# Optimization experiments

Measured on AMD Instinct MI355X. Metric: run time of the kernel, lower is better.

## Reference

```python
import jax, jax.numpy as jnp
import numpy as np

FISTA_ITER = 50
LAMBDA = 0.1
POWER_ITER = 100


def power_method(W):
    # Estimates c = largest eigenvalue of W^T W (squared spectral norm).
    # Torch code uses a random init vector; we use a fixed key for determinism.
    X0 = jax.random.normal(jax.random.key(1), (1, W.shape[1]), dtype=W.dtype)

    def body(i, carry):
        X, _ = carry
        X = (X @ W.T) @ W            # [1, m]
        nm = jnp.linalg.norm(X)
        return (X / nm, nm)

    _, nm = jax.lax.fori_loop(0, POWER_ITER, body, (X0, jnp.asarray(1.0, W.dtype)))
    return nm


def soft_threshold(X, lam):
    return jnp.sign(X) * jax.nn.relu(jnp.abs(X) - lam)


def fista(Y, W, lam, iters):
    c = power_method(W)
    eta = 1.0 / c
    Gamma0 = soft_threshold(Y @ (eta * W), lam)   # [B, m]
    Y_norm = jnp.linalg.norm(Y)
    t0 = jnp.asarray(1.0, Y.dtype)

    def step(carry, _):
        Gamma, Z, t = carry
        residual = Z @ W.T - Y                                   # [B, n]
        Gamma_new = soft_threshold(Z - eta * (residual @ W), lam / c)
        t_new = (1.0 + jnp.sqrt(1.0 + 4.0 * t ** 2)) / 2.0
        Z_new = Gamma_new + (t - 1.0) / t_new * (Gamma_new - Gamma)
        nrm = jnp.linalg.norm(residual) / Y_norm
        return (Gamma_new, Z_new, t_new), nrm

    (Gamma, _, _), norms = jax.lax.scan(step, (Gamma0, Gamma0, t0), None, length=iters)
    return Gamma, norms


def setup_inputs() -> dict:
    key = jax.random.key(0)
    k1, k2 = jax.random.split(key)
    Y = jax.random.normal(k1, (8192, 784), dtype=jnp.float32)
    W = jax.random.normal(k2, (784, 2048), dtype=jnp.float32)
    W = W / jnp.linalg.norm(W, axis=0, keepdims=True)  # NormDict
    return {"Y": Y, "W": W}


def reference(Y, W):
    Gamma, norms = fista(Y, W, LAMBDA, FISTA_ITER)
    X = Gamma @ W.T                  # reconstruction [B, 784]
    return (X, Gamma, norms)
```

## Files before the change

### kernel.cpp

```cpp
#include <hip/hip_runtime.h>
#include <math.h>

#define B_DIM   8192
#define N_DIM   784
#define NPAD    800
#define NROWS_W 896
#define M_DIM   2048
#define XSZ     (B_DIM*N_DIM)
#define GSZ     (B_DIM*M_DIM)
#define NITER   50
#define PITER   100

typedef __attribute__((ext_vector_type(8))) short short8;
typedef __attribute__((ext_vector_type(4))) float floatx4;

__device__ __forceinline__ void async_ld16(const unsigned short* g, unsigned short* l){
  __builtin_amdgcn_global_load_lds(
      (const __attribute__((address_space(1))) unsigned int*)g,
      (__attribute__((address_space(3))) unsigned int*)l,
      16, 0, 0);
}

__device__ __forceinline__ unsigned rotl32(unsigned x, int d){ return (x<<d)|(x>>(32-d)); }

__device__ void threefry2x32(unsigned& v0, unsigned& v1){
  const unsigned ks0=0u, ks1=1u, ks2=0x1BD11BDBu;
  unsigned x0=v0+ks0, x1=v1+ks1;
#define RND(R) { x0+=x1; x1=rotl32(x1,R); x1^=x0; }
  RND(13) RND(15) RND(26) RND(6)
  x0+=ks1; x1+=ks2+1u;
  RND(17) RND(29) RND(16) RND(24)
  x0+=ks2; x1+=ks0+2u;
  RND(13) RND(15) RND(26) RND(6)
  x0+=ks0; x1+=ks1+3u;
  RND(17) RND(29) RND(16) RND(24)
  x0+=ks1; x1+=ks2+4u;
  RND(13) RND(15) RND(26) RND(6)
  x0+=ks2; x1+=ks0+5u;
#undef RND
  v0=x0; v1=x1;
}

__device__ float erfinv_f(float x){
  float w = -logf((1.0f-x)*(1.0f+x));
  float p;
  if (w < 5.0f){
    w -= 2.5f;
    p = 2.81022636e-08f;
    p = fmaf(p,w, 3.43273939e-07f);
    p = fmaf(p,w,-3.5233877e-06f);
    p = fmaf(p,w,-4.39150654e-06f);
    p = fmaf(p,w, 0.00021858087f);
    p = fmaf(p,w,-0.00125372503f);
    p = fmaf(p,w,-0.00417768164f);
    p = fmaf(p,w, 0.246640727f);
    p = fmaf(p,w, 1.50140941f);
  } else {
    w = sqrtf(w) - 3.0f;
    p = -0.000200214257f;
    p = fmaf(p,w, 0.000100950558f);
    p = fmaf(p,w, 0.00134934322f);
    p = fmaf(p,w,-0.00367342844f);
    p = fmaf(p,w, 0.00573950773f);
    p = fmaf(p,w,-0.0076224613f);
    p = fmaf(p,w, 0.00943887047f);
    p = fmaf(p,w, 1.00167406f);
    p = fmaf(p,w, 2.83297682f);
  }
  return p*x;
}

__device__ float bits_to_normal(unsigned b){
  unsigned fb = (b>>9) | 0x3f800000u;
  float u01 = __uint_as_float(fb) - 1.0f;
  const float lo = -0.99999994f;
  float u = u01*(1.0f - lo) + lo;
  u = fmaxf(lo, u);
  return 1.41421356237f * erfinv_f(u);
}

__global__ void setup_kernel(float* __restrict__ xbuf0, float* __restrict__ accs){
  int i = threadIdx.x;
  if (i < 64) accs[i] = 0.0f;
  unsigned v0 = (unsigned)i, v1 = (unsigned)(1024+i);
  threefry2x32(v0, v1);
  xbuf0[i]        = bits_to_normal(v0);
  xbuf0[1024 + i] = bits_to_normal(v1);
}

__device__ __forceinline__ unsigned short f2bf(float f){
  unsigned u = __float_as_uint(f);
  unsigned r = (u + 0x7fffu + ((u>>16)&1u)) >> 16;
  return (unsigned short)r;
}
__device__ __forceinline__ unsigned pack2(float a, float b){
  return (unsigned)f2bf(a) | ((unsigned)f2bf(b) << 16);
}
__device__ __forceinline__ float bf2f(unsigned short s){
  return __uint_as_float(((unsigned)s) << 16);
}

__global__ void conv_w(const float* __restrict__ W, unsigned short* __restrict__ Wbf){
  int i4 = (blockIdx.x*256 + threadIdx.x)*4;
  int row = i4 >> 11;
  uint2 p = make_uint2(0,0);
  if (row < N_DIM){
    float4 v = *(const float4*)(W + (size_t)row*M_DIM + (i4 & 2047));
    p.x = pack2(v.x, v.y); p.y = pack2(v.z, v.w);
  }
  *(uint2*)(Wbf + i4) = p;
}

__global__ void conv_y(const float* __restrict__ Y, unsigned short* __restrict__ Ybf){
  int row = blockIdx.x;
  int c4 = threadIdx.x*4;
  if (c4 >= NPAD) return;
  uint2 p = make_uint2(0,0);
  if (c4 < N_DIM){
    float4 v = *(const float4*)(Y + (size_t)row*N_DIM + c4);
    p.x = pack2(v.x, v.y); p.y = pack2(v.z, v.w);
  }
  *(uint2*)(Ybf + (size_t)row*NPAD + c4) = p;
}

__global__ void transpose_w(const float* __restrict__ W, unsigned short* __restrict__ WTbf){
  __shared__ float tile[32][33];
  int k0 = blockIdx.x*32;
  int j0 = blockIdx.y*32;
  int tx = threadIdx.x & 31, ty = threadIdx.x >> 5;
#pragma unroll
  for (int i=0;i<4;i++){
    int j = j0 + ty + 8*i;
    float v = (j < N_DIM) ? W[(size_t)j*M_DIM + k0 + tx] : 0.0f;
    tile[tx][ty+8*i] = v;
  }
  __syncthreads();
#pragma unroll
  for (int i=0;i<4;i++){
    int k = k0 + ty + 8*i;
    WTbf[(size_t)k*NPAD + j0 + tx] = f2bf(tile[ty+8*i][tx]);
  }
}

__global__ __launch_bounds__(256)
void compute_q(const float* __restrict__ W, float* __restrict__ Q){
  __shared__ float As2[16][132];
  __shared__ float Bs2[16][132];
  const int t = threadIdx.x;
  const int a0 = blockIdx.x*128, b0 = blockIdx.y*128;
  const int ty = t>>4, tx = t&15;
  float acc[8][8];
#pragma unroll
  for (int i=0;i<8;i++)
#pragma unroll
    for (int j=0;j<8;j++) acc[i][j]=0.0f;

  for (int j0=0; j0<N_DIM; j0+=16){
#pragma unroll
    for (int h=0; h<8; ++h){
      int idx = h*256 + t;
      int r = idx>>7, c = idx&127;
      As2[r][c] = W[(size_t)(j0+r)*M_DIM + a0 + c];
      Bs2[r][c] = W[(size_t)(j0+r)*M_DIM + b0 + c];
    }
    __syncthreads();
#pragma unroll
    for (int kk=0; kk<16; ++kk){
      float a[8], b[8];
#pragma unroll
      for (int i=0;i<8;i++) a[i] = As2[kk][ty*8+i];
#pragma unroll
      for (int j=0;j<8;j++) b[j] = Bs2[kk][tx*8+j];
#pragma unroll
      for (int i=0;i<8;i++)
#pragma unroll
        for (int j=0;j<8;j++) acc[i][j] = fmaf(a[i], b[j], acc[i][j]);
    }
    __syncthreads();
  }
#pragma unroll
  for (int i=0;i<8;i++){
    int a = a0 + ty*8 + i;
#pragma unroll
    for (int j=0;j<8;j++) Q[(size_t)a*M_DIM + b0 + tx*8 + j] = acc[i][j];
  }
}

__global__ void sumsq_kernel(const float* __restrict__ v, int n, float* __restrict__ acc){
  __shared__ float red[256];
  int t = threadIdx.x;
  float s = 0.0f;
  for (int i = blockIdx.x*256 + t; i < n; i += gridDim.x*256){ float x = v[i]; s = fmaf(x,x,s); }
  red[t] = s; __syncthreads();
  for (int off=128; off>0; off>>=1){ if (t<off) red[t]+=red[t+off]; __syncthreads(); }
  if (t==0) atomicAdd(acc, red[0]);
}

__global__ void pm_q(const float* __restrict__ x, const float* __restrict__ Q,
                     float* __restrict__ xout){
  __shared__ float red[256];
  int t = threadIdx.x;
  float s = 0.0f;
  for (int k=t; k<M_DIM; k+=256){ float v = x[k]; s = fmaf(v,v,s); }
  red[t]=s; __syncthreads();
  for (int off=128; off>0; off>>=1){ if (t<off) red[t]+=red[t+off]; __syncthreads(); }
  float inv = 1.0f/sqrtf(red[0]);
  int wave = t>>6, lane = t&63;
  int j = blockIdx.x*4 + wave;
  const float* Qr = Q + (size_t)j*M_DIM;
  float acc = 0.0f;
  for (int k=lane; k<M_DIM; k+=64) acc = fmaf(x[k], Qr[k], acc);
  for (int off=32; off>0; off>>=1) acc += __shfl_down(acc, off);
  if (lane==0) xout[j] = acc * inv;
}

__global__ void finish_power(const float* __restrict__ xfin, const float* __restrict__ accs,
                             float* __restrict__ params){
  __shared__ float red[256];
  int t = threadIdx.x;
  float s = 0.0f;
  for (int k=t; k<M_DIM; k+=256){ float v = xfin[k]; s = fmaf(v,v,s); }
  red[t]=s; __syncthreads();
  for (int off=128; off>0; off>>=1){ if (t<off) red[t]+=red[t+off]; __syncthreads(); }
  if (t==0){
    float c = sqrtf(red[0]);
    params[0] = c;
    params[1] = 1.0f/c;
    params[2] = 0.1f/c;
    params[3] = sqrtf(accs[0]);
  }
}

__device__ __forceinline__ float softthr(float v, float th){
  float a = fmaxf(fabsf(v) - th, 0.0f);
  return copysignf(a, v);
}

template<int MODE>
__global__ __launch_bounds__(256)
void mfma_nt(const unsigned short* __restrict__ Abf,
             const unsigned short* __restrict__ Bbf,
             const float* __restrict__ Y,
             unsigned short* __restrict__ Rbf,
             float* __restrict__ X,
             float* __restrict__ nacc){
  __shared__ float4 smem4[1024];
  unsigned short* As = (unsigned short*)smem4;
  unsigned short* Bs = As + 64*32;
  float* fbuf = (float*)smem4;

  const int bid = blockIdx.x;
  const int g8  = bid & 7, w = bid >> 3;
  const int mt  = w / 7, nt = w - mt*7;
  const int m0  = (g8*16 + mt)*64;
  const int n0  = nt*128;

  const int t    = threadIdx.x;
  const int wave = t>>6, lane = t&63;
  const int wm2  = wave>>1, wn2 = wave&1;
  const int quad = lane>>4, l15 = lane&15;
  const int lrow = lane>>2;
  const int lk   = (lane&3)*8;

  floatx4 acc[2][4];
#pragma unroll
  for (int i=0;i<2;i++)
#pragma unroll
    for (int j=0;j<4;j++) acc[i][j] = (floatx4)(0.0f);

  for (int k0=0; k0<M_DIM; k0+=32){
    async_ld16(Abf + (size_t)(m0 + wave*16 + lrow)*M_DIM + k0 + lk, &As[wave*512]);
#pragma unroll
    for (int c=0; c<2; ++c){
      int chunk = wave*2 + c;
      async_ld16(Bbf + (size_t)(n0 + chunk*16 + lrow)*M_DIM + k0 + lk, &Bs[chunk*512]);
    }
    __syncthreads();
    short8 af[2], bfr[4];
#pragma unroll
    for (int ti=0; ti<2; ++ti)
      af[ti] = *(const short8*)&As[(wm2*32 + ti*16 + l15)*32 + quad*8];
#pragma unroll
    for (int tj=0; tj<4; ++tj)
      bfr[tj] = *(const short8*)&Bs[(wn2*64 + tj*16 + l15)*32 + quad*8];
#pragma unroll
    for (int ti=0; ti<2; ++ti)
#pragma unroll
      for (int tj=0; tj<4; ++tj)
        acc[ti][tj] = __builtin_amdgcn_mfma_f32_16x16x32_bf16(af[ti], bfr[tj], acc[ti][tj], 0, 0, 0);
    __syncthreads();
  }

  float ss = 0.0f;
#pragma unroll
  for (int c=0; c<2; ++c){
    if (wn2 == c){
#pragma unroll
      for (int ti=0; ti<2; ++ti)
#pragma unroll
        for (int tj=0; tj<4; ++tj)
#pragma unroll
          for (int r=0; r<4; ++r)
            fbuf[(wm2*32 + ti*16 + quad*4 + r)*64 + tj*16 + l15] = acc[ti][tj][r];
    }
    __syncthreads();
#pragma unroll
    for (int k=0; k<4; ++k){
      int row = k*16 + (t>>4);
      int col = (t&15)*4;
      int m = m0 + row;
      int n = n0 + c*64 + col;
      float4 v = *(const float4*)&fbuf[row*64 + col];
      if (MODE==0){
        if (n < N_DIM){
          float4 yv = *(const float4*)(Y + (size_t)m*N_DIM + n);
          float r0 = v.x - yv.x, r1 = v.y - yv.y, r2 = v.z - yv.z, r3 = v.w - yv.w;
          uint2 p; p.x = pack2(r0, r1); p.y = pack2(r2, r3);
          *(uint2*)(Rbf + (size_t)m*NPAD + n) = p;
          ss = fmaf(r0,r0, fmaf(r1,r1, fmaf(r2,r2, fmaf(r3,r3, ss))));
        } else if (n < NPAD){
          *(uint2*)(Rbf + (size_t)m*NPAD + n) = make_uint2(0,0);
        }
      } else {
        if (n < N_DIM) *(float4*)(X + (size_t)m*N_DIM + n) = v;
      }
    }
    __syncthreads();
  }

  if (MODE==0){
    for (int off=32; off>0; off>>=1) ss += __shfl_down(ss, off);
    if (lane==0) atomicAdd(nacc, ss);
  }
}

template<int MODE>
__global__ __launch_bounds__(256)
void mfma_nn(const unsigned short* __restrict__ Abf,
             const unsigned short* __restrict__ WTbf,
             float* __restrict__ Gamma,
             unsigned short* __restrict__ Zhi,
             unsigned short* __restrict__ Zlo,
             const float* __restrict__ params,
             float mu){
  __shared__ float4 smem4[1024];
  unsigned short* As = (unsigned short*)smem4;
  unsigned short* Bs = As + 128*32;
  float* fbuf = (float*)smem4;

  const int bid = blockIdx.x;
  const int g8  = bid & 7, w = bid >> 3;
  const int m0  = (g8*8 + (w>>4))*128;
  const int n0  = (w & 15)*128;

  const int t    = threadIdx.x;
  const int wave = t>>6, lane = t&63;
  const int wm   = wave>>1, wn = wave&1;
  const int quad = lane>>4, l15 = lane&15;
  const int ch0  = wave*2;
  const int lrow = lane>>2;
  const int lk   = (lane&3)*8;

  floatx4 acc[4][4];
#pragma unroll
  for (int i=0;i<4;i++)
#pragma unroll
    for (int j=0;j<4;j++) acc[i][j] = (floatx4)(0.0f);

  for (int k0=0; k0<NPAD; k0+=32){
#pragma unroll
    for (int c=0; c<2; ++c){
      int chunk = ch0 + c;
      async_ld16(Abf  + (size_t)(m0 + chunk*16 + lrow)*NPAD + k0 + lk, &As[chunk*512]);
      async_ld16(WTbf + (size_t)(n0 + chunk*16 + lrow)*NPAD + k0 + lk, &Bs[chunk*512]);
    }
    __syncthreads();
    short8 af[4], bfr[4];
#pragma unroll
    for (int ti=0; ti<4; ++ti)
      af[ti] = *(const short8*)&As[(wm*64 + ti*16 + l15)*32 + quad*8];
#pragma unroll
    for (int tj=0; tj<4; ++tj)
      bfr[tj] = *(const short8*)&Bs[(wn*64 + tj*16 + l15)*32 + quad*8];
#pragma unroll
    for (int ti=0; ti<4; ++ti)
#pragma unroll
      for (int tj=0; tj<4; ++tj)
        acc[ti][tj] = __builtin_amdgcn_mfma_f32_16x16x32_bf16(af[ti], bfr[tj], acc[ti][tj], 0, 0, 0);
    __syncthreads();
  }

  const float eta  = params[1];
  const float lamc = params[2];

#pragma unroll
  for (int c=0; c<4; ++c){
    if (wn == (c>>1)){
      int tjb = (c&1)*2;
#pragma unroll
      for (int ti=0; ti<4; ++ti)
#pragma unroll
        for (int u=0; u<2; ++u)
#pragma unroll
          for (int r=0; r<4; ++r)
            fbuf[(wm*64 + ti*16 + quad*4 + r)*32 + u*16 + l15] = acc[ti][tjb+u][r];
    }
    __syncthreads();
#pragma unroll
    for (int k=0; k<4; ++k){
      int row = k*32 + (t>>3);
      int col = (t&7)*4;
      int m = m0 + row;
      int n = n0 + c*32 + col;
      size_t idx = (size_t)m*M_DIM + n;
      float4 g4 = *(const float4*)&fbuf[row*32 + col];
      float gr[4] = {g4.x, g4.y, g4.z, g4.w};
      float go4[4];
      if (MODE!=0){
        uint2 ph = *(const uint2*)(Zhi + idx);
        uint2 pl = *(const uint2*)(Zlo + idx);
        unsigned short h[4] = {(unsigned short)(ph.x&0xffff),(unsigned short)(ph.x>>16),
                               (unsigned short)(ph.y&0xffff),(unsigned short)(ph.y>>16)};
        unsigned short l[4] = {(unsigned short)(pl.x&0xffff),(unsigned short)(pl.x>>16),
                               (unsigned short)(pl.y&0xffff),(unsigned short)(pl.y>>16)};
        float4 gov = *(const float4*)(Gamma + idx);
        go4[0]=gov.x; go4[1]=gov.y; go4[2]=gov.z; go4[3]=gov.w;
#pragma unroll
        for (int e=0;e<4;e++){
          float zv = bf2f(h[e]) + bf2f(l[e]);
          gr[e] = softthr(zv - eta*gr[e], lamc);
        }
      } else {
#pragma unroll
        for (int e=0;e<4;e++) gr[e] = softthr(eta*gr[e], 0.1f);
      }
      *(float4*)(Gamma + idx) = make_float4(gr[0],gr[1],gr[2],gr[3]);
      if (MODE==1){
        float zn[4];
#pragma unroll
        for (int e=0;e<4;e++) zn[e] = gr[e] + mu*(gr[e] - go4[e]);
        unsigned short h0=f2bf(zn[0]), h1=f2bf(zn[1]), h2=f2bf(zn[2]), h3=f2bf(zn[3]);
        uint2 ph; ph.x = (unsigned)h0 | ((unsigned)h1<<16); ph.y = (unsigned)h2 | ((unsigned)h3<<16);
        uint2 pl; pl.x = pack2(zn[0]-bf2f(h0), zn[1]-bf2f(h1));
                  pl.y = pack2(zn[2]-bf2f(h2), zn[3]-bf2f(h3));
        *(uint2*)(Zhi + idx) = ph;
        *(uint2*)(Zlo + idx) = pl;
      } else if (MODE==0){
        unsigned short h0=f2bf(gr[0]), h1=f2bf(gr[1]), h2=f2bf(gr[2]), h3=f2bf(gr[3]);
        uint2 ph; ph.x = (unsigned)h0 | ((unsigned)h1<<16); ph.y = (unsigned)h2 | ((unsigned)h3<<16);
        uint2 pl; pl.x = pack2(gr[0]-bf2f(h0), gr[1]-bf2f(h1));
                  pl.y = pack2(gr[2]-bf2f(h2), gr[3]-bf2f(h3));
        *(uint2*)(Zhi + idx) = ph;
        *(uint2*)(Zlo + idx) = pl;
      } else {
        uint2 ph; ph.x = pack2(gr[0], gr[1]); ph.y = pack2(gr[2], gr[3]);
        *(uint2*)(Zhi + idx) = ph;
      }
    }
    __syncthreads();
  }
}

__global__ void norms_finalize(const float* __restrict__ nacc, const float* __restrict__ params,
                               float* __restrict__ out){
  int i = threadIdx.x;
  if (i < NITER) out[i] = sqrtf(nacc[i]) / params[3];
}

extern "C" void kernel_launch(void* const* d_in, const int* in_sizes, int n_in,
                              void* d_out, int out_size, void* d_ws, size_t ws_size,
                              hipStream_t stream){
  const float* Y  = (const float*)d_in[0];
  const float* W  = (const float*)d_in[1];
  float* out      = (float*)d_out;
  float* X        = out;
  float* Gamma    = out + XSZ;
  float* norms    = out + XSZ + GSZ;

  unsigned short* Zhi  = (unsigned short*)d_ws;
  unsigned short* Zlo  = Zhi  + (size_t)GSZ;
  unsigned short* Rbf  = Zlo  + (size_t)GSZ;
  unsigned short* Wbf  = Rbf  + (size_t)B_DIM*NPAD;
  unsigned short* WTbf = Wbf  + (size_t)NROWS_W*M_DIM;
  float* Q      = (float*)(WTbf + (size_t)M_DIM*NPAD);
  float* xb0    = Q + (size_t)M_DIM*M_DIM;
  float* xb1    = xb0 + M_DIM;
  float* params = xb1 + M_DIM;
  float* accs   = params + 8;

  setup_kernel<<<dim3(1), dim3(1024), 0, stream>>>(xb0, accs);
  sumsq_kernel<<<dim3(512), dim3(256), 0, stream>>>(Y, XSZ, accs);
  conv_w      <<<dim3(1792), dim3(256), 0, stream>>>(W, Wbf);
  transpose_w <<<dim3(64,25), dim3(256), 0, stream>>>(W, WTbf);
  conv_y      <<<dim3(B_DIM), dim3(256), 0, stream>>>(Y, Rbf);

  compute_q<<<dim3(16,16), dim3(256), 0, stream>>>(W, Q);
  float* xa = xb0; float* xc = xb1;
  for (int it=0; it<PITER; ++it){
    pm_q<<<dim3(512), dim3(256), 0, stream>>>(xa, Q, xc);
    float* tmp = xa; xa = xc; xc = tmp;
  }
  finish_power<<<dim3(1), dim3(256), 0, stream>>>(xa, accs, params);

  mfma_nn<0><<<dim3(1024), dim3(256), 0, stream>>>(Rbf, WTbf, Gamma, Zhi, Zlo, params, 0.0f);

  float tcur = 1.0f;
  for (int it=0; it<NITER; ++it){
    mfma_nt<0><<<dim3(896), dim3(256), 0, stream>>>(Zhi, Wbf, Y, Rbf, nullptr, accs + 1 + it);
    float tsq = tcur*tcur;
    float tn  = (1.0f + sqrtf(1.0f + 4.0f*tsq)) / 2.0f;
    float mu  = (tcur - 1.0f) / tn;
    tcur = tn;
    if (it < NITER-1)
      mfma_nn<1><<<dim3(1024), dim3(256), 0, stream>>>(Rbf, WTbf, Gamma, Zhi, Zlo, params, mu);
    else
      mfma_nn<2><<<dim3(1024), dim3(256), 0, stream>>>(Rbf, WTbf, Gamma, Zhi, Zlo, params, mu);
  }

  norms_finalize<<<dim3(1), dim3(64), 0, stream>>>(accs + 1, params, norms);

  mfma_nt<1><<<dim3(896), dim3(256), 0, stream>>>(Zhi, Wbf, nullptr, nullptr, X, nullptr);
}
```

Measured before the change: 9.500 ms.

## Square the Gram matrix for power iteration and narrow mfma_nn tiles

Computes Q² = (WᵀW)² once and runs the power method with half as many matrix-vector launches, bracketed by single Q applications. Separately, shrinks the FISTA gradient GEMM tile from 128x128 to 128x64, doubling the grid and requesting higher occupancy via launch bounds. The squaring adds a large fp32 SIMT GEMM up front and slightly changes iteration count and normalization; the smaller tile lowers per-block reuse in exchange for more parallelism.

Measured after the change: 9.727 ms. +2.4%, slower.

```diff
diff --git a/kernel.cpp b/kernel.cpp
--- a/kernel.cpp
+++ b/kernel.cpp
@@ -142,8 +142,9 @@
   }
 }
 
+template<int KROWS>
 __global__ __launch_bounds__(256)
-void compute_q(const float* __restrict__ W, float* __restrict__ Q){
+void compute_qk(const float* __restrict__ A, float* __restrict__ Qout){
   __shared__ float As2[16][132];
   __shared__ float Bs2[16][132];
   const int t = threadIdx.x;
@@ -155,13 +156,13 @@
 #pragma unroll
     for (int j=0;j<8;j++) acc[i][j]=0.0f;
 
-  for (int j0=0; j0<N_DIM; j0+=16){
+  for (int j0=0; j0<KROWS; j0+=16){
 #pragma unroll
     for (int h=0; h<8; ++h){
       int idx = h*256 + t;
       int r = idx>>7, c = idx&127;
-      As2[r][c] = W[(size_t)(j0+r)*M_DIM + a0 + c];
-      Bs2[r][c] = W[(size_t)(j0+r)*M_DIM + b0 + c];
+      As2[r][c] = A[(size_t)(j0+r)*M_DIM + a0 + c];
+      Bs2[r][c] = A[(size_t)(j0+r)*M_DIM + b0 + c];
     }
     __syncthreads();
 #pragma unroll
@@ -182,7 +183,7 @@
   for (int i=0;i<8;i++){
     int a = a0 + ty*8 + i;
 #pragma unroll
-    for (int j=0;j<8;j++) Q[(size_t)a*M_DIM + b0 + tx*8 + j] = acc[i][j];
+    for (int j=0;j<8;j++) Qout[(size_t)a*M_DIM + b0 + tx*8 + j] = acc[i][j];
   }
 }
 
@@ -196,7 +197,7 @@
   if (t==0) atomicAdd(acc, red[0]);
 }
 
-__global__ void pm_q(const float* __restrict__ x, const float* __restrict__ Q,
+__global__ void pm_q(const float* __restrict__ x, const float* __restrict__ M,
                      float* __restrict__ xout){
   __shared__ float red[256];
   int t = threadIdx.x;
@@ -207,9 +208,9 @@
   float inv = 1.0f/sqrtf(red[0]);
   int wave = t>>6, lane = t&63;
   int j = blockIdx.x*4 + wave;
-  const float* Qr = Q + (size_t)j*M_DIM;
+  const float* Mr = M + (size_t)j*M_DIM;
   float acc = 0.0f;
-  for (int k=lane; k<M_DIM; k+=64) acc = fmaf(x[k], Qr[k], acc);
+  for (int k=lane; k<M_DIM; k+=64) acc = fmaf(x[k], Mr[k], acc);
   for (int off=32; off>0; off>>=1) acc += __shfl_down(acc, off);
   if (lane==0) xout[j] = acc * inv;
 }
@@ -335,7 +336,7 @@
 }
 
 template<int MODE>
-__global__ __launch_bounds__(256)
+__global__ __launch_bounds__(256, 5)
 void mfma_nn(const unsigned short* __restrict__ Abf,
              const unsigned short* __restrict__ WTbf,
              float* __restrict__ Gamma,
@@ -350,42 +351,41 @@
 
   const int bid = blockIdx.x;
   const int g8  = bid & 7, w = bid >> 3;
-  const int m0  = (g8*8 + (w>>4))*128;
-  const int n0  = (w & 15)*128;
+  const int m0  = (g8*8 + (w>>5))*128;
+  const int n0  = (w & 31)*64;
 
   const int t    = threadIdx.x;
   const int wave = t>>6, lane = t&63;
   const int wm   = wave>>1, wn = wave&1;
   const int quad = lane>>4, l15 = lane&15;
-  const int ch0  = wave*2;
   const int lrow = lane>>2;
   const int lk   = (lane&3)*8;
 
-  floatx4 acc[4][4];
+  floatx4 acc[4][2];
 #pragma unroll
   for (int i=0;i<4;i++)
 #pragma unroll
-    for (int j=0;j<4;j++) acc[i][j] = (floatx4)(0.0f);
+    for (int j=0;j<2;j++) acc[i][j] = (floatx4)(0.0f);
 
   for (int k0=0; k0<NPAD; k0+=32){
 #pragma unroll
     for (int c=0; c<2; ++c){
-      int chunk = ch0 + c;
-      async_ld16(Abf  + (size_t)(m0 + chunk*16 + lrow)*NPAD + k0 + lk, &As[chunk*512]);
-      async_ld16(WTbf + (size_t)(n0 + chunk*16 + lrow)*NPAD + k0 + lk, &Bs[chunk*512]);
-    }
-    __syncthreads();
-    short8 af[4], bfr[4];
+      int chunk = wave*2 + c;
+      async_ld16(Abf + (size_t)(m0 + chunk*16 + lrow)*NPAD + k0 + lk, &As[chunk*512]);
+    }
+    async_ld16(WTbf + (size_t)(n0 + wave*16 + lrow)*NPAD + k0 + lk, &Bs[wave*512]);
+    __syncthreads();
+    short8 af[4], bfr[2];
 #pragma unroll
     for (int ti=0; ti<4; ++ti)
       af[ti] = *(const short8*)&As[(wm*64 + ti*16 + l15)*32 + quad*8];
 #pragma unroll
-    for (int tj=0; tj<4; ++tj)
-      bfr[tj] = *(const short8*)&Bs[(wn*64 + tj*16 + l15)*32 + quad*8];
+    for (int tj=0; tj<2; ++tj)
+      bfr[tj] = *(const short8*)&Bs[(wn*32 + tj*16 + l15)*32 + quad*8];
 #pragma unroll
     for (int ti=0; ti<4; ++ti)
 #pragma unroll
-      for (int tj=0; tj<4; ++tj)
+      for (int tj=0; tj<2; ++tj)
         acc[ti][tj] = __builtin_amdgcn_mfma_f32_16x16x32_bf16(af[ti], bfr[tj], acc[ti][tj], 0, 0, 0);
     __syncthreads();
   }
@@ -394,16 +394,15 @@
   const float lamc = params[2];
 
 #pragma unroll
-  for (int c=0; c<4; ++c){
-    if (wn == (c>>1)){
-      int tjb = (c&1)*2;
+  for (int c=0; c<2; ++c){
+    if (wn == c){
 #pragma unroll
       for (int ti=0; ti<4; ++ti)
 #pragma unroll
         for (int u=0; u<2; ++u)
 #pragma unroll
           for (int r=0; r<4; ++r)
-            fbuf[(wm*64 + ti*16 + quad*4 + r)*32 + u*16 + l15] = acc[ti][tjb+u][r];
+            fbuf[(wm*64 + ti*16 + quad*4 + r)*32 + u*16 + l15] = acc[ti][u][r];
     }
     __syncthreads();
 #pragma unroll
@@ -483,7 +482,8 @@
   unsigned short* Wbf  = Rbf  + (size_t)B_DIM*NPAD;
   unsigned short* WTbf = Wbf  + (size_t)NROWS_W*M_DIM;
   float* Q      = (float*)(WTbf + (size_t)M_DIM*NPAD);
-  float* xb0    = Q + (size_t)M_DIM*M_DIM;
+  float* Q2     = Q + (size_t)M_DIM*M_DIM;
+  float* xb0    = Q2 + (size_t)M_DIM*M_DIM;
   float* xb1    = xb0 + M_DIM;
   float* params = xb1 + M_DIM;
   float* accs   = params + 8;
@@ -494,15 +494,18 @@
   transpose_w <<<dim3(64,25), dim3(256), 0, stream>>>(W, WTbf);
   conv_y      <<<dim3(B_DIM), dim3(256), 0, stream>>>(Y, Rbf);
 
-  compute_q<<<dim3(16,16), dim3(256), 0, stream>>>(W, Q);
-  float* xa = xb0; float* xc = xb1;
-  for (int it=0; it<PITER; ++it){
-    pm_q<<<dim3(512), dim3(256), 0, stream>>>(xa, Q, xc);
+  compute_qk<N_DIM><<<dim3(16,16), dim3(256), 0, stream>>>(W, Q);
+  compute_qk<M_DIM><<<dim3(16,16), dim3(256), 0, stream>>>(Q, Q2);
+  pm_q<<<dim3(512), dim3(256), 0, stream>>>(xb0, Q, xb1);
+  float* xa = xb1; float* xc = xb0;
+  for (int it=0; it<49; ++it){
+    pm_q<<<dim3(512), dim3(256), 0, stream>>>(xa, Q2, xc);
     float* tmp = xa; xa = xc; xc = tmp;
   }
-  finish_power<<<dim3(1), dim3(256), 0, stream>>>(xa, accs, params);
-
-  mfma_nn<0><<<dim3(1024), dim3(256), 0, stream>>>(Rbf, WTbf, Gamma, Zhi, Zlo, params, 0.0f);
+  pm_q<<<dim3(512), dim3(256), 0, stream>>>(xa, Q, xc);
+  finish_power<<<dim3(1), dim3(256), 0, stream>>>(xc, accs, params);
+
+  mfma_nn<0><<<dim3(2048), dim3(256), 0, stream>>>(Rbf, WTbf, Gamma, Zhi, Zlo, params, 0.0f);
 
   float tcur = 1.0f;
   for (int it=0; it<NITER; ++it){
@@ -512,9 +515,9 @@
     float mu  = (tcur - 1.0f) / tn;
     tcur = tn;
     if (it < NITER-1)
-      mfma_nn<1><<<dim3(1024), dim3(256), 0, stream>>>(Rbf, WTbf, Gamma, Zhi, Zlo, params, mu);
+      mfma_nn<1><<<dim3(2048), dim3(256), 0, stream>>>(Rbf, WTbf, Gamma, Zhi, Zlo, params, mu);
     else
-      mfma_nn<2><<<dim3(1024), dim3(256), 0, stream>>>(Rbf, WTbf, Gamma, Zhi, Zlo, params, mu);
+      mfma_nn<2><<<dim3(2048), dim3(256), 0, stream>>>(Rbf, WTbf, Gamma, Zhi, Zlo, params, mu);
   }
 
   norms_finalize<<<dim3(1), dim3(64), 0, stream>>>(accs + 1, params, norms);
```
